# Performance work log

Hardware: AMD Instinct MI355X
Metric: run time of the kernel (lower is better)

Reference implementation:

```python
import jax, jax.numpy as jnp
import numpy as np

B, S, H = 64, 512, 1024  # batch, seq_len, hidden (input_size == hidden_size per source)


def setup_inputs() -> dict:
    key = jax.random.key(0)
    k1, k2 = jax.random.split(key)
    x = jax.random.normal(k1, (B, S, H), dtype=jnp.float32)
    # xavier_uniform_ for U: bound = sqrt(6/(fan_in+fan_out))
    bound = float(np.sqrt(6.0 / (H + 4 * H)))
    U = jax.random.uniform(k2, (H, 4 * H), dtype=jnp.float32, minval=-bound, maxval=bound)
    bias = jnp.zeros((4 * H,), dtype=jnp.float32)
    return {"x": x, "U": U, "bias": bias}


def reference(x, U, bias):
    # Faithful LSTM recurrence (peephole=False; note: W is declared in the
    # original module but never used in forward, and the gate matmul uses U
    # on the input x_t, exactly as in the source).
    batch = x.shape[0]
    HS = U.shape[0]
    h0 = jnp.zeros((batch, HS), dtype=x.dtype)
    c0 = jnp.zeros((batch, HS), dtype=x.dtype)

    def step(carry, x_t):
        h_t, c_t = carry
        gates = x_t @ U + bias  # [B, 4H]
        i_t = jax.nn.sigmoid(gates[:, :HS])
        f_t = jax.nn.sigmoid(gates[:, HS:2 * HS])
        g_t = jnp.tanh(gates[:, 2 * HS:3 * HS])
        o_t = jax.nn.sigmoid(gates[:, 3 * HS:])
        c_t = f_t * c_t + i_t * g_t
        h_t = o_t * jnp.tanh(c_t)
        return (h_t, c_t), h_t

    (h_T, c_T), hs = jax.lax.scan(step, (h0, c0), jnp.swapaxes(x, 0, 1))  # hs: [S, B, H]
    hidden_sequence = jnp.swapaxes(hs, 0, 1)  # [B, S, H]
    return hidden_sequence, (h_T, c_T)
```

## Files before the change

kernel.cpp:

```cpp
#include <hip/hip_runtime.h>
#include <hip/hip_bf16.h>
#include <stdint.h>

typedef __bf16 bf16x8 __attribute__((ext_vector_type(8)));
typedef float  f32x4  __attribute__((ext_vector_type(4)));
typedef unsigned short u16x8 __attribute__((ext_vector_type(8)));
typedef unsigned short u16x4 __attribute__((ext_vector_type(4)));
typedef _Float16 f16x4 __attribute__((ext_vector_type(4)));

#define HS    1024
#define FOURH 4096
#define SEQ   512
#define BATCH 64

#define BAR()  asm volatile("s_barrier" ::: "memory")
#define VMW(n) asm volatile("s_waitcnt vmcnt(" #n ")" ::: "memory")

__device__ __forceinline__ unsigned short f2bf(float f) {
    unsigned u = __builtin_bit_cast(unsigned, f);
    u = (u + 0x7FFFu + ((u >> 16) & 1u)) >> 16;
    return (unsigned short)u;
}

__device__ __forceinline__ void gload_lds16(const void* g, void* l) {
    __builtin_amdgcn_global_load_lds(
        (const __attribute__((address_space(1))) void*)g,
        (__attribute__((address_space(3))) void*)l, 16, 0, 0);
}

__device__ __forceinline__ float fsigmoid(float v) {
    return __builtin_amdgcn_rcpf(1.f + __expf(-v));
}
__device__ __forceinline__ float ftanh(float v) {
    return 1.f - 2.f * __builtin_amdgcn_rcpf(1.f + __expf(2.f * v));
}

__global__ __launch_bounds__(256) void convert_x(const float* __restrict__ x,
                                                 unsigned short* __restrict__ xb,
                                                 long n8) {
    long i = (long)blockIdx.x * blockDim.x + threadIdx.x;
    long stride = (long)gridDim.x * blockDim.x;
    for (; i < n8; i += stride) {
        const float4* p = (const float4*)(x + i * 8);
        float4 a = p[0], b = p[1];
        u16x8 o;
        o[0] = f2bf(a.x); o[1] = f2bf(a.y); o[2] = f2bf(a.z); o[3] = f2bf(a.w);
        o[4] = f2bf(b.x); o[5] = f2bf(b.y); o[6] = f2bf(b.z); o[7] = f2bf(b.w);
        *(u16x8*)(xb + i * 8) = o;
    }
}

__global__ __launch_bounds__(256) void transpose_u(const float* __restrict__ U,
                                                   unsigned short* __restrict__ Ut) {
    __shared__ float tile[32][33];
    int bx = blockIdx.x;
    int tn = bx >> 5;
    int tk = bx & 31;
    int c = threadIdx.x & 31;
    int r = threadIdx.x >> 5;
#pragma unroll
    for (int i = 0; i < 4; ++i) {
        int k = tk * 32 + r + i * 8;
        tile[r + i * 8][c] = U[(size_t)k * FOURH + tn * 32 + c];
    }
    __syncthreads();
#pragma unroll
    for (int i = 0; i < 4; ++i) {
        int nl = r + i * 8;
        int n = tn * 32 + nl;
        int gate = n >> 10, h = n & 1023;
        int pn = ((h >> 4) << 6) | (gate << 4) | (h & 15);
        Ut[(size_t)pn * HS + tk * 32 + c] = f2bf(tile[c][nl]);
    }
}

__global__ __launch_bounds__(512, 1) void gemm_gates8(
    const unsigned short* __restrict__ Xb,
    const unsigned short* __restrict__ Ut,
    const float* __restrict__ bias,
    _Float16* __restrict__ gates,
    int lg2chunk, int s0) {
    __shared__ unsigned short LDSU[65536];

    int nwg = gridDim.x;
    int bid = blockIdx.x;
    int wg = (bid & 7) * (nwg >> 3) + (bid >> 3);
    int mt = wg >> 4;
    int nt = wg & 15;

    int tid = threadIdx.x;
    int w = tid >> 6, l = tid & 63;
    int wr = w >> 2, wc = w & 3;
    int lr = l & 15, lg = l >> 4;

    const int m0 = mt * 256, n0 = nt * 256;
    const int cmask = (1 << lg2chunk) - 1;

    const int rdo = lr * 32 + ((lg * 8) ^ ((lr & 8) << 1));
    const int srow = l >> 2;
    const int skin = ((l & 3) * 8) ^ (((l >> 5) & 1) << 4);

    const unsigned short* pAq[4];
    const unsigned short* pBq[4];
#pragma unroll
    for (int q = 0; q < 4; ++q) {
        int rowg = q * 64 + (w >> 1) * 16 + srow;
        int mrow = m0 + rowg;
        int b = mrow >> lg2chunk, sl2 = mrow & cmask;
        pAq[q] = Xb + (size_t)(b * SEQ + s0 + sl2) * HS + (w & 1) * 32 + skin;
        pBq[q] = Ut + (size_t)(n0 + rowg) * HS + (w & 1) * 32 + skin;
    }
    const int dsub = (w >> 1) * 2 + (w & 1);

    f32x4 acc[8][4];
#pragma unroll
    for (int mi = 0; mi < 8; ++mi)
#pragma unroll
        for (int ni = 0; ni < 4; ++ni) acc[mi][ni] = 0.f;

#define SA(T, Q) gload_lds16(pAq[Q] + (T) * 64, \
        &LDSU[(((T) & 1) << 15) + ((Q) * 8 + dsub) * 512])
#define SB(T, Q) gload_lds16(pBq[Q] + (T) * 64, \
        &LDSU[(((T) & 1) << 15) + 16384 + ((Q) * 8 + dsub) * 512])

    bf16x8 aq[2][4], bn0[2][2], bn1[2][2];

#define RDA(MH) \
    _Pragma("unroll") for (int ks = 0; ks < 2; ++ks) \
    _Pragma("unroll") for (int mi = 0; mi < 4; ++mi) \
        aq[ks][mi] = *(const bf16x8*)(buf + ((wr * 8 + (MH) * 4 + mi) * 2 + ks) * 512 + rdo)
#define RDB(NH, BN) \
    _Pragma("unroll") for (int ks = 0; ks < 2; ++ks) \
    _Pragma("unroll") for (int ni = 0; ni < 2; ++ni) \
        BN[ks][ni] = *(const bf16x8*)(buf + 16384 + ((wc * 4 + (NH) * 2 + ni) * 2 + ks) * 512 + rdo)
#define MMQ(MH, NH, BN) \
    __builtin_amdgcn_s_setprio(1); \
    _Pragma("unroll") for (int ks = 0; ks < 2; ++ks) \
    _Pragma("unroll") for (int mi = 0; mi < 4; ++mi) \
    _Pragma("unroll") for (int ni = 0; ni < 2; ++ni) \
        acc[(MH) * 4 + mi][(NH) * 2 + ni] = __builtin_amdgcn_mfma_f32_16x16x32_bf16( \
            aq[ks][mi], BN[ks][ni], acc[(MH) * 4 + mi][(NH) * 2 + ni], 0, 0, 0); \
    __builtin_amdgcn_s_setprio(0)

    SA(0, 0); SA(0, 2); SB(0, 0); SB(0, 1); SB(0, 2); SB(0, 3); SA(0, 1); SA(0, 3);
    VMW(2); BAR();

    for (int t = 0; t < 16; ++t) {
        const unsigned short* buf = &LDSU[(t & 1) << 15];
        RDA(0);
        RDB(0, bn0);
        if (t < 15) { SA(t + 1, 0); SA(t + 1, 2); }
        MMQ(0, 0, bn0);
        RDB(1, bn1);
        if (t < 15) { SB(t + 1, 0); SB(t + 1, 1); SB(t + 1, 2); SB(t + 1, 3); }
        MMQ(0, 1, bn1);
        if (t < 15) { VMW(6); } else { VMW(0); }
        BAR();
        RDA(1);
        if (t < 15) { SA(t + 1, 1); SA(t + 1, 3); }
        MMQ(1, 1, bn1);
        MMQ(1, 0, bn0);
        if (t < 15) { VMW(2); }
        BAR();
    }

    const int hh = ((n0 >> 6) + wc) * 16 + lr;
    const float bi = bias[hh], bf = bias[1024 + hh];
    const float bg = bias[2048 + hh], bo = bias[3072 + hh];
#pragma unroll
    for (int mi = 0; mi < 8; ++mi) {
        size_t rg = (size_t)(((m0 + wr * 128 + mi * 16) >> 2) + lg);
        u16x4 pkP, pkF, pkO;
#pragma unroll
        for (int r = 0; r < 4; ++r) {
            float iv = fsigmoid(acc[mi][0][r] + bi);
            float fv = fsigmoid(acc[mi][1][r] + bf);
            float gv = ftanh(acc[mi][2][r] + bg);
            float ov = fsigmoid(acc[mi][3][r] + bo);
            float pv = iv * gv;
            pkP[r] = __builtin_bit_cast(unsigned short, (_Float16)pv);
            pkF[r] = __builtin_bit_cast(unsigned short, (_Float16)fv);
            pkO[r] = __builtin_bit_cast(unsigned short, (_Float16)ov);
        }
        _Float16* gp = gates + rg * 12288 + hh * 4;
        *(u16x4*)(gp)        = pkP;
        *(u16x4*)(gp + 4096) = pkF;
        *(u16x4*)(gp + 8192) = pkO;
    }
#undef SA
#undef SB
#undef RDA
#undef RDB
#undef MMQ
}

__global__ __launch_bounds__(256) void lstm_recur(
    const _Float16* __restrict__ gates,
    float* __restrict__ out,
    float* __restrict__ cstate,
    int chunk, int s0) {
    int t = blockIdx.x * 256 + threadIdx.x;
    int b = t >> 10, h = t & 1023;
    float c = (s0 == 0) ? 0.f : cstate[t];
    const _Float16* gp = gates + (size_t)((b * chunk) >> 2) * 12288 + h * 4;
    float* op = out + (size_t)(b * SEQ + s0) * HS + h;
    float hv = 0.f;
    const int ng = chunk >> 2;
    int g4 = 0;
    for (; g4 + 1 < ng; g4 += 2) {
        f16x4 pv[2], fv[2], ov[2];
#pragma unroll
        for (int u = 0; u < 2; ++u) {
            const _Float16* q = gp + (size_t)(g4 + u) * 12288;
            pv[u] = *(const f16x4*)(q);
            fv[u] = *(const f16x4*)(q + 4096);
            ov[u] = *(const f16x4*)(q + 8192);
        }
#pragma unroll
        for (int u = 0; u < 2; ++u) {
#pragma unroll
            for (int r = 0; r < 4; ++r) {
                c = (float)fv[u][r] * c + (float)pv[u][r];
                float th = ftanh(c);
                hv = (float)ov[u][r] * th;
                op[(size_t)((g4 + u) * 4 + r) * HS] = hv;
            }
        }
    }
    for (; g4 < ng; ++g4) {
        const _Float16* q = gp + (size_t)g4 * 12288;
        f16x4 pv = *(const f16x4*)(q);
        f16x4 fv = *(const f16x4*)(q + 4096);
        f16x4 ov = *(const f16x4*)(q + 8192);
#pragma unroll
        for (int r = 0; r < 4; ++r) {
            c = (float)fv[r] * c + (float)pv[r];
            float th = ftanh(c);
            hv = (float)ov[r] * th;
            op[(size_t)(g4 * 4 + r) * HS] = hv;
        }
    }
    cstate[t] = c;
    if (s0 + chunk == SEQ) {
        out[(size_t)BATCH * SEQ * HS + t] = hv;
        out[(size_t)BATCH * SEQ * HS + BATCH * HS + t] = c;
    }
}

extern "C" void kernel_launch(void* const* d_in, const int* in_sizes, int n_in,
                              void* d_out, int out_size, void* d_ws, size_t ws_size,
                              hipStream_t stream) {
    const float* x    = (const float*)d_in[0];
    const float* U    = (const float*)d_in[1];
    const float* bias = (const float*)d_in[2];
    float* out = (float*)d_out;
    char*  ws  = (char*)d_ws;

    unsigned short* Xb = (unsigned short*)ws;
    unsigned short* Ut = (unsigned short*)(ws + 67108864);
    float* cstate      = (float*)(ws + 75497472);
    _Float16* gates    = (_Float16*)(ws + 75759616);
    const size_t fixed = 75759616;

    int chunk = 512;
    while (chunk > 4 && fixed + (size_t)BATCH * chunk * 6144 > ws_size)
        chunk >>= 1;
    int lg2 = 31 - __builtin_clz(chunk);

    convert_x<<<2048, 256, 0, stream>>>(x, Xb, (long)BATCH * SEQ * HS / 8);
    transpose_u<<<4096, 256, 0, stream>>>(U, Ut);

    for (int s0 = 0; s0 < SEQ; s0 += chunk) {
        int mtiles = (BATCH * chunk) / 256;
        gemm_gates8<<<mtiles * 16, 512, 0, stream>>>(Xb, Ut, bias, gates, lg2, s0);
        lstm_recur<<<256, 256, 0, stream>>>(gates, out, cstate, chunk, s0);
    }
}
```

Baseline: 376.7 us.

## Restructure gate GEMM to 16 waves per block with 64x64 warp tiles

The gate GEMM moves from 8 waves with 128x64 per-wave tiles to 16 waves of 1024 threads, each owning a 64x64 sub-tile with half the accumulators. The load pipeline is rebuilt: every wave loads one A and one B row-slice per K-half, and the prefetch of the next half-step interleaves across the two LDS buffers. The aim is more latency hiding and lower register pressure per wave, at the cost of more LDS read traffic per MFMA and more barrier participants. The launch bounds hint at 4 blocks per CU, which the 128KB LDS per block makes unlikely.

Measured after the change: 406.9 us. +8.0%, slower.

```diff
diff --git a/kernel.cpp b/kernel.cpp
--- a/kernel.cpp
+++ b/kernel.cpp
@@ -74,7 +74,7 @@
     }
 }
 
-__global__ __launch_bounds__(512, 1) void gemm_gates8(
+__global__ __launch_bounds__(1024, 4) void gemm_gates16(
     const unsigned short* __restrict__ Xb,
     const unsigned short* __restrict__ Ut,
     const float* __restrict__ bias,
@@ -100,81 +100,71 @@
     const int srow = l >> 2;
     const int skin = ((l & 3) * 8) ^ (((l >> 5) & 1) << 4);
 
-    const unsigned short* pAq[4];
-    const unsigned short* pBq[4];
-#pragma unroll
-    for (int q = 0; q < 4; ++q) {
-        int rowg = q * 64 + (w >> 1) * 16 + srow;
-        int mrow = m0 + rowg;
+    const unsigned short* pA;
+    const unsigned short* pB;
+    {
+        int mrow = m0 + w * 16 + srow;
         int b = mrow >> lg2chunk, sl2 = mrow & cmask;
-        pAq[q] = Xb + (size_t)(b * SEQ + s0 + sl2) * HS + (w & 1) * 32 + skin;
-        pBq[q] = Ut + (size_t)(n0 + rowg) * HS + (w & 1) * 32 + skin;
-    }
-    const int dsub = (w >> 1) * 2 + (w & 1);
-
-    f32x4 acc[8][4];
-#pragma unroll
-    for (int mi = 0; mi < 8; ++mi)
+        pA = Xb + (size_t)(b * SEQ + s0 + sl2) * HS + skin;
+        pB = Ut + (size_t)(n0 + w * 16 + srow) * HS + skin;
+    }
+
+    f32x4 acc[4][4];
+#pragma unroll
+    for (int mi = 0; mi < 4; ++mi)
 #pragma unroll
         for (int ni = 0; ni < 4; ++ni) acc[mi][ni] = 0.f;
 
-#define SA(T, Q) gload_lds16(pAq[Q] + (T) * 64, \
-        &LDSU[(((T) & 1) << 15) + ((Q) * 8 + dsub) * 512])
-#define SB(T, Q) gload_lds16(pBq[Q] + (T) * 64, \
-        &LDSU[(((T) & 1) << 15) + 16384 + ((Q) * 8 + dsub) * 512])
-
-    bf16x8 aq[2][4], bn0[2][2], bn1[2][2];
-
-#define RDA(MH) \
-    _Pragma("unroll") for (int ks = 0; ks < 2; ++ks) \
+#define SG(T, KS) { \
+    gload_lds16(pA + (T) * 64 + (KS) * 32, \
+        &LDSU[(((T) & 1) << 15) + (w * 2 + (KS)) * 512]); \
+    gload_lds16(pB + (T) * 64 + (KS) * 32, \
+        &LDSU[(((T) & 1) << 15) + 16384 + (w * 2 + (KS)) * 512]); }
+
+    bf16x8 av[4], bv[4];
+
+#define RDA(KS) \
     _Pragma("unroll") for (int mi = 0; mi < 4; ++mi) \
-        aq[ks][mi] = *(const bf16x8*)(buf + ((wr * 8 + (MH) * 4 + mi) * 2 + ks) * 512 + rdo)
-#define RDB(NH, BN) \
-    _Pragma("unroll") for (int ks = 0; ks < 2; ++ks) \
-    _Pragma("unroll") for (int ni = 0; ni < 2; ++ni) \
-        BN[ks][ni] = *(const bf16x8*)(buf + 16384 + ((wc * 4 + (NH) * 2 + ni) * 2 + ks) * 512 + rdo)
-#define MMQ(MH, NH, BN) \
+        av[mi] = *(const bf16x8*)(buf + (((wr * 4 + mi) * 2) + (KS)) * 512 + rdo)
+#define RDB(KS) \
+    _Pragma("unroll") for (int ni = 0; ni < 4; ++ni) \
+        bv[ni] = *(const bf16x8*)(buf + 16384 + (((wc * 4 + ni) * 2) + (KS)) * 512 + rdo)
+#define MMQ() \
     __builtin_amdgcn_s_setprio(1); \
-    _Pragma("unroll") for (int ks = 0; ks < 2; ++ks) \
     _Pragma("unroll") for (int mi = 0; mi < 4; ++mi) \
-    _Pragma("unroll") for (int ni = 0; ni < 2; ++ni) \
-        acc[(MH) * 4 + mi][(NH) * 2 + ni] = __builtin_amdgcn_mfma_f32_16x16x32_bf16( \
-            aq[ks][mi], BN[ks][ni], acc[(MH) * 4 + mi][(NH) * 2 + ni], 0, 0, 0); \
+    _Pragma("unroll") for (int ni = 0; ni < 4; ++ni) \
+        acc[mi][ni] = __builtin_amdgcn_mfma_f32_16x16x32_bf16( \
+            av[mi], bv[ni], acc[mi][ni], 0, 0, 0); \
     __builtin_amdgcn_s_setprio(0)
 
-    SA(0, 0); SA(0, 2); SB(0, 0); SB(0, 1); SB(0, 2); SB(0, 3); SA(0, 1); SA(0, 3);
+    SG(0, 0); SG(0, 1); SG(1, 0);
     VMW(2); BAR();
 
     for (int t = 0; t < 16; ++t) {
         const unsigned short* buf = &LDSU[(t & 1) << 15];
-        RDA(0);
-        RDB(0, bn0);
-        if (t < 15) { SA(t + 1, 0); SA(t + 1, 2); }
-        MMQ(0, 0, bn0);
-        RDB(1, bn1);
-        if (t < 15) { SB(t + 1, 0); SB(t + 1, 1); SB(t + 1, 2); SB(t + 1, 3); }
-        MMQ(0, 1, bn1);
-        if (t < 15) { VMW(6); } else { VMW(0); }
+        RDA(0); RDB(0);
+        if (t < 15) SG(t + 1, 1);
+        MMQ();
+        if (t < 15) { VMW(2); } else { VMW(0); }
         BAR();
-        RDA(1);
-        if (t < 15) { SA(t + 1, 1); SA(t + 1, 3); }
-        MMQ(1, 1, bn1);
-        MMQ(1, 0, bn0);
-        if (t < 15) { VMW(2); }
+        RDA(1); RDB(1);
+        if (t < 14) SG(t + 2, 0);
+        MMQ();
+        if (t < 14) { VMW(2); }
         BAR();
     }
 
     const int hh = ((n0 >> 6) + wc) * 16 + lr;
-    const float bi = bias[hh], bf = bias[1024 + hh];
+    const float bi = bias[hh], bf_ = bias[1024 + hh];
     const float bg = bias[2048 + hh], bo = bias[3072 + hh];
 #pragma unroll
-    for (int mi = 0; mi < 8; ++mi) {
-        size_t rg = (size_t)(((m0 + wr * 128 + mi * 16) >> 2) + lg);
+    for (int mi = 0; mi < 4; ++mi) {
+        size_t rg = (size_t)(((m0 + wr * 64 + mi * 16) >> 2) + lg);
         u16x4 pkP, pkF, pkO;
 #pragma unroll
         for (int r = 0; r < 4; ++r) {
             float iv = fsigmoid(acc[mi][0][r] + bi);
-            float fv = fsigmoid(acc[mi][1][r] + bf);
+            float fv = fsigmoid(acc[mi][1][r] + bf_);
             float gv = ftanh(acc[mi][2][r] + bg);
             float ov = fsigmoid(acc[mi][3][r] + bo);
             float pv = iv * gv;
@@ -187,8 +177,7 @@
         *(u16x4*)(gp + 4096) = pkF;
         *(u16x4*)(gp + 8192) = pkO;
     }
-#undef SA
-#undef SB
+#undef SG
 #undef RDA
 #undef RDB
 #undef MMQ
@@ -272,7 +261,7 @@
 
     for (int s0 = 0; s0 < SEQ; s0 += chunk) {
         int mtiles = (BATCH * chunk) / 256;
-        gemm_gates8<<<mtiles * 16, 512, 0, stream>>>(Xb, Ut, bias, gates, lg2, s0);
+        gemm_gates16<<<mtiles * 16, 1024, 0, stream>>>(Xb, Ut, bias, gates, lg2, s0);
         lstm_recur<<<256, 256, 0, stream>>>(gates, out, cstate, chunk, s0);
     }
 }
```
